# Optimization experiments

Measured on AMD Instinct MI355X. Metric: run time of the kernel, lower is better.

Reference implementation:

```python
import jax, jax.numpy as jnp
import numpy as np

NH, NG, NR = 128, 32, 15
NT, NS = 730, 800


def _linear_init(k, fan_in, fan_out):
    k1, k2 = jax.random.split(k)
    lim = 1.0 / np.sqrt(fan_in)
    w = jax.random.uniform(k1, (fan_in, fan_out), jnp.float32, -lim, lim)
    b = jax.random.uniform(k2, (fan_out,), jnp.float32, -lim, lim)
    return w, b


def _mlp(x, w1, b1, w2, b2):
    # Linear -> Tanh -> (Dropout: identity in eval) -> Linear
    return jnp.tanh(x @ w1 + b1) @ w2 + b2


def setup_inputs() -> dict:
    key = jax.random.key(0)
    ks = jax.random.split(key, 8)
    x = jax.random.normal(ks[0], (NT, NS, 6), jnp.float32)
    xc = jax.random.normal(ks[1], (NS, NG), jnp.float32)
    fcW1_w, fcW1_b = _linear_init(ks[2], NG, 256)
    fcW2_w, fcW2_b = _linear_init(ks[3], 256, NH * 7)
    fcT1_w, fcT1_b = _linear_init(ks[4], 6 + NG, 256)
    fcT2_w, fcT2_b = _linear_init(ks[5], 256, NH * 3)
    fcR1_w, fcR1_b = _linear_init(ks[6], NG, 256)
    fcR2_w, fcR2_b = _linear_init(ks[7], 256, NH * NR)
    return dict(x=x, xc=xc,
                fcW1_w=fcW1_w, fcW1_b=fcW1_b, fcW2_w=fcW2_w, fcW2_b=fcW2_b,
                fcT1_w=fcT1_w, fcT1_b=fcT1_b, fcT2_w=fcT2_w, fcT2_b=fcT2_b,
                fcR1_w=fcR1_w, fcR1_b=fcR1_b, fcR2_w=fcR2_w, fcR2_b=fcR2_b)


def _waternet(x, xc, fcW1_w, fcW1_b, fcW2_w, fcW2_b,
              fcT1_w, fcT1_b, fcT2_w, fcT2_b, fcR1_w, fcR1_b, fcR2_w, fcR2_b):
    nh, nr = NH, NR
    nt, ns, _ = x.shape
    P, E, T1, T2 = x[..., 0], x[..., 1], x[..., 2], x[..., 3]

    # static parameter head: [ns, nh*7] split into 7 physical params (sepPar)
    w = _mlp(xc, fcW1_w, fcW1_b, fcW2_w, fcW2_b)
    sig = jax.nn.sigmoid
    kp = sig(w[:, 0 * nh:1 * nh])
    ks_ = sig(w[:, 1 * nh:2 * nh])
    kg = sig(w[:, 2 * nh:3 * nh]) / 10.0
    gp = sig(w[:, 3 * nh:4 * nh])
    gL = jnp.exp(w[:, 4 * nh:5 * nh]) * 2.0
    qb = jax.nn.relu(w[:, 5 * nh:6 * nh])
    ga = jax.nn.softmax(w[:, 6 * nh:7 * nh], axis=1)

    # time-varying head on [forcings ; tiled static attrs]
    xcT = jnp.concatenate([x, jnp.broadcast_to(xc[None], (nt, ns, xc.shape[-1]))], axis=-1)
    v = _mlp(xcT, fcT1_w, fcT1_b, fcT2_w, fcT2_b)  # [nt, ns, nh*3]
    # vi = hardsigmoid(2*v) = clip((2v+3)/6, 0, 1) = clip(v/3 + 0.5, 0, 1)
    vi = jnp.clip(v[..., :nh] / 3.0 + 0.5, 0.0, 1.0)
    ve = jax.nn.relu(v[..., nh:2 * nh]) * 2.0
    vm = jnp.exp(v[..., 2 * nh:3 * nh])

    wR = _mlp(xc, fcR1_w, fcR1_b, fcR2_w, fcR2_b)  # [ns, nh*nr]

    # snow fraction vf = arccos((T1+T2)/(T2-T1))/pi, clamped by temperature masks
    denom = T2 - T1
    cf = (T1 + T2) / jnp.where(denom == 0.0, 1.0, denom)
    vf = jnp.arccos(jnp.clip(cf, -0.999999, 0.999999)) / 3.1415
    vf = jnp.where(T1 >= 0.0, 0.0, vf)
    vf = jnp.where(T2 <= 0.0, 1.0, vf)

    Ps = P * vf                                 # [nt, ns] snow
    Pl = (P * (1.0 - vf))[..., None] * vi       # [nt, ns, nh] liquid
    Ev = E[..., None] * ve                      # [nt, ns, nh]

    def step(carry, inp):
        Sf, Ss, Sg = carry
        ps, pl, ev, vmk = inp
        qf = jnp.minimum(Sf + ps[:, None], vmk)
        Sf = jax.nn.relu(Sf + ps[:, None] - vmk)
        H = jax.nn.relu(Ss + pl + qf - ev)
        qp = jax.nn.relu(kp * (H - gL))
        qs = ks_ * jnp.minimum(H, gL)
        Ss = H - qp - qs
        qsg = qs * gp
        qg = kg * (Sg + qsg) + qb
        Sg = Sg - qg
        # routing conv and final ga-sum are linear, so route qp+qso+qg together
        return (Sf, Ss, Sg), qp + qs * (1.0 - gp) + qg

    z = jnp.zeros((ns, nh), x.dtype)
    _, QT = jax.lax.scan(step, (z, z, z), (Ps, Pl, Ev, vm))  # QT: [nt, ns, nh]

    # convTS: per-(site, bucket) causal FIR routing with kernel r [ns, nh, nr]
    r = jax.nn.relu(wR).reshape(ns, nh, nr)
    xpad = jnp.pad(QT, ((nr - 1, 0), (0, 0), (0, 0)))
    QR = jnp.zeros_like(QT)
    for i in range(nr):  # small fixed nr taps
        QR = QR + xpad[nr - 1 - i:nr - 1 - i + nt] * r[:, :, i]

    return jnp.sum(QR * ga, axis=2)  # [nt, ns]


def reference(x, xc, fcW1_w, fcW1_b, fcW2_w, fcW2_b,
              fcT1_w, fcT1_b, fcT2_w, fcT2_b, fcR1_w, fcR1_b, fcR2_w, fcR2_b):
    return _waternet(x, xc, fcW1_w, fcW1_b, fcW2_w, fcW2_b,
                     fcT1_w, fcT1_b, fcT2_w, fcT2_b, fcR1_w, fcR1_b, fcR2_w, fcR2_b)
```

## Files before the change

### kernel.cpp

```cpp
#include <hip/hip_runtime.h>
#include <cmath>

#define NHID 128
#define NSITE 800
#define NTIME 730
#define NRTAP 15
constexpr int NSH = NSITE * NHID;

typedef _Float16 f16x8 __attribute__((ext_vector_type(8)));
typedef _Float16 f16x2 __attribute__((ext_vector_type(2)));
typedef float f32x4 __attribute__((ext_vector_type(4)));

__device__ __forceinline__ float tanh_fast(float x) {
    float e = __expf(2.0f * x);
    return 1.0f - 2.0f / (e + 1.0f);
}
__device__ __forceinline__ float sigmoid_fast(float x) {
    return 1.0f / (1.0f + __expf(-x));
}
__device__ __forceinline__ unsigned short h_bits(_Float16 h) {
    union { _Float16 h; unsigned short u; } c; c.h = h; return c.u;
}
__device__ __forceinline__ void unpack_h2(unsigned u, float& a, float& b) {
    union { unsigned u; f16x2 h; } cv; cv.u = u;
    a = (float)cv.h.x; b = (float)cv.h.y;
}
__device__ __forceinline__ int ah_swz(int jg, int r) {
    return jg * 64 + ((r & ~7) | ((r ^ jg) & 7));
}

__global__ void k_prep_w2h(const float* __restrict__ w2, _Float16* __restrict__ w2s)
{
    int idx = blockIdx.x * 256 + threadIdx.x;
    if (idx >= 98304) return;
    int k = idx / 384, col = idx - k * 384;
    int K0 = k >> 5, kg = (k >> 3) & 3, e = k & 7;
    w2s[(size_t)K0 * 12288 + kg * 3072 + col * 8 + e] = (_Float16)w2[(size_t)k * 384 + col];
}

__global__ void k_site_l1(const float* __restrict__ xc,
                          const float* __restrict__ w1W, const float* __restrict__ b1W,
                          const float* __restrict__ w1R, const float* __restrict__ b1R,
                          const float* __restrict__ w1T, const float* __restrict__ b1T,
                          float* __restrict__ h1w, float* __restrict__ h1r,
                          float* __restrict__ basec)
{
    __shared__ float xr[32];
    int s = blockIdx.x, j = threadIdx.x;
    if (j < 32) xr[j] = xc[s * 32 + j];
    __syncthreads();
    float aW = b1W[j], aR = b1R[j], aT = b1T[j];
#pragma unroll 8
    for (int k = 0; k < 32; ++k) {
        float xv = xr[k];
        aW = fmaf(xv, w1W[k * 256 + j], aW);
        aR = fmaf(xv, w1R[k * 256 + j], aR);
        aT = fmaf(xv, w1T[(6 + k) * 256 + j], aT);
    }
    h1w[s * 256 + j]   = tanh_fast(aW);
    h1r[s * 256 + j]   = tanh_fast(aR);
    basec[s * 256 + j] = aT;
}

__global__ void k_whead(const float* __restrict__ h1w,
                        const float* __restrict__ w2, const float* __restrict__ b2,
                        float* __restrict__ params)
{
    __shared__ float h[8 * 256];
    int sBase = blockIdx.x * 8, g = blockIdx.y, tid = threadIdx.x;
    for (int p = tid; p < 2048; p += 128) h[p] = h1w[sBase * 256 + p];
    __syncthreads();
    float bias = b2[g * 128 + tid];
    float acc[8];
#pragma unroll
    for (int i = 0; i < 8; ++i) acc[i] = bias;
    for (int k = 0; k < 256; ++k) {
        float wv = w2[k * 896 + g * 128 + tid];
#pragma unroll
        for (int i = 0; i < 8; ++i) acc[i] = fmaf(h[i * 256 + k], wv, acc[i]);
    }
#pragma unroll
    for (int i = 0; i < 8; ++i) {
        float v = acc[i], o;
        if (g == 0 || g == 1 || g == 3)  o = sigmoid_fast(v);
        else if (g == 2)                 o = sigmoid_fast(v) * 0.1f;
        else if (g == 4)                 o = __expf(v) * 2.0f;
        else if (g == 5)                 o = fmaxf(v, 0.0f);
        else                             o = v;
        params[g * NSH + (sBase + i) * 128 + tid] = o;
    }
}

__global__ void k_softmax_ga(float* __restrict__ ga)
{
    int s = blockIdx.x, h = threadIdx.x;
    float v = ga[s * 128 + h];
    float m = v;
#pragma unroll
    for (int off = 32; off; off >>= 1) m = fmaxf(m, __shfl_xor(m, off));
    __shared__ float ra[2], rb[2];
    if ((h & 63) == 0) ra[h >> 6] = m;
    __syncthreads();
    m = fmaxf(ra[0], ra[1]);
    float e = __expf(v - m);
    float t = e;
#pragma unroll
    for (int off = 32; off; off >>= 1) t += __shfl_xor(t, off);
    if ((h & 63) == 0) rb[h >> 6] = t;
    __syncthreads();
    ga[s * 128 + h] = e / (rb[0] + rb[1]);
}

__global__ void k_rhead(const float* __restrict__ h1r,
                        const float* __restrict__ w2, const float* __restrict__ b2,
                        float* __restrict__ rbuf)
{
    __shared__ float h[8 * 256];
    int sBase = blockIdx.x * 8, g = blockIdx.y, tid = threadIdx.x;
    for (int p = tid; p < 2048; p += 128) h[p] = h1r[sBase * 256 + p];
    __syncthreads();
    int c = g * 128 + tid;
    float bias = b2[c];
    float acc[8];
#pragma unroll
    for (int i = 0; i < 8; ++i) acc[i] = bias;
    for (int k = 0; k < 256; ++k) {
        float wv = w2[k * 1920 + c];
#pragma unroll
        for (int i = 0; i < 8; ++i) acc[i] = fmaf(h[i * 256 + k], wv, acc[i]);
    }
    int hh = c / 15, ii = c - hh * 15;
#pragma unroll
    for (int i = 0; i < 8; ++i)
        rbuf[ii * NSH + (sBase + i) * 128 + hh] = fmaxf(acc[i], 0.0f);
}

struct ThSm3 {
    f16x8 Ah[2048];
    float xt[64][6];
    float pls[64], evs[64], psv[64];
};

__global__ __launch_bounds__(512, 2) void k_combo6(
    const float* __restrict__ x, const float* __restrict__ w1T,
    const float* __restrict__ basec, const f16x8* __restrict__ w2B,
    const float* __restrict__ b2,
    const float* __restrict__ params, const float* __restrict__ rbuf,
    float* __restrict__ state, float* __restrict__ fut, float* __restrict__ out,
    unsigned* __restrict__ PVw, float* __restrict__ PSw, int t0h, int rowsH,
    const unsigned* __restrict__ PVr, const float* __restrict__ PSr,
    int t0s, int Tcs, int isFirst, int nScan)
{
    __shared__ __align__(16) char smem[sizeof(ThSm3)];
    int tid = threadIdx.x;

    if ((int)blockIdx.x < nScan) {
        float* part = (float*)smem;
        int sl = tid >> 7, hc = tid & 127;
        int lane = tid & 63, wid = tid >> 6;
        int site = blockIdx.x * 4 + sl;
        int cell = site * 128 + hc;

        float kp  = params[0 * NSH + cell];
        float ksP = params[1 * NSH + cell];
        float kgP = params[2 * NSH + cell];
        float gp  = params[3 * NSH + cell];
        float gL  = params[4 * NSH + cell];
        float qb  = params[5 * NSH + cell];
        float ga  = params[6 * NSH + cell];
        float kq  = ksP * (1.0f - gp);

        float wr[NRTAP];
#pragma unroll
        for (int i = 0; i < NRTAP; ++i) wr[i] = ga * rbuf[i * NSH + cell];

        float Sf, Ss, Sg, f[NRTAP];
        if (isFirst) {
            Sf = Ss = Sg = 0.0f;
#pragma unroll
            for (int i = 0; i < NRTAP; ++i) f[i] = 0.0f;
        } else {
            Sf = state[cell];
            Ss = state[NSH + cell];
            Sg = state[2 * NSH + cell];
#pragma unroll
            for (int i = 0; i < NRTAP; ++i) f[i] = fut[i * NSH + cell];
        }

        const unsigned* pvp = PVr + cell;

#define LD_T(PV_, PS_, T_) { int t_ = (T_); bool ok_ = t_ < Tcs;               \
        PV_ = ok_ ? pvp[(size_t)t_ * NSH] : 0u;                                \
        PS_ = ok_ ? PSr[(size_t)t_ * 800 + site] : 0.0f; }

        unsigned pvA[4], pvB[4], pvC[4], pvD[4];
        float psA[4], psB[4], psC[4], psD[4];
#pragma unroll
        for (int i = 0; i < 4; ++i) LD_T(pvA[i], psA[i], i)
#pragma unroll
        for (int i = 0; i < 4; ++i) LD_T(pvB[i], psB[i], 4 + i)
#pragma unroll
        for (int i = 0; i < 4; ++i) LD_T(pvC[i], psC[i], 8 + i)
#pragma unroll
        for (int i = 0; i < 4; ++i) LD_T(pvD[i], psD[i], 12 + i)

        int ngroups = (Tcs + 3) >> 2;
        for (int g = 0; g < ngroups; ++g) {
            int tb = g * 4;
            unsigned pvE[4]; float psE[4];
#pragma unroll
            for (int i = 0; i < 4; ++i) LD_T(pvE[i], psE[i], tb + 16 + i)

            float cs[4];
#pragma unroll
            for (int i = 0; i < 4; ++i) {
                cs[i] = 0.0f;
                if (tb + i < Tcs) {
                    float dlt, vm;
                    unpack_h2(pvA[i], dlt, vm);
                    float ps = psA[i];

                    float x1 = Sf + ps;
                    float qf = fminf(x1, vm);
                    Sf = fmaxf(x1 - vm, 0.0f);
                    float H  = fmaxf(Ss + qf + dlt, 0.0f);
                    float qp = fmaxf(kp * (H - gL), 0.0f);
                    float mh = fminf(H, gL);
                    float qs = ksP * mh;
                    Ss = H - qp - qs;
                    float qg = fmaf(kgP, fmaf(qs, gp, Sg), qb);
                    Sg = Sg - qg;
                    float qt = qp + kq * mh + qg;
#pragma unroll
                    for (int j = 0; j < NRTAP; ++j) f[j] = fmaf(wr[j], qt, f[j]);
                    cs[i] = f[0];
#pragma unroll
                    for (int j = 0; j < NRTAP - 1; ++j) f[j] = f[j + 1];
                    f[NRTAP - 1] = 0.0f;
                }
            }
#pragma unroll
            for (int i = 0; i < 4; ++i) {
                float c = cs[i];
#pragma unroll
                for (int off = 32; off; off >>= 1) c += __shfl_xor(c, off);
                cs[i] = c;
            }
            if (lane == 0) {
#pragma unroll
                for (int i = 0; i < 4; ++i)
                    if (tb + i < Tcs) part[wid * 128 + tb + i] = cs[i];
            }
#pragma unroll
            for (int i = 0; i < 4; ++i) {
                pvA[i] = pvB[i]; pvB[i] = pvC[i]; pvC[i] = pvD[i]; pvD[i] = pvE[i];
                psA[i] = psB[i]; psB[i] = psC[i]; psC[i] = psD[i]; psD[i] = psE[i];
            }
        }
#undef LD_T

        state[cell]           = Sf;
        state[NSH + cell]     = Ss;
        state[2 * NSH + cell] = Sg;
#pragma unroll
        for (int i = 0; i < NRTAP; ++i) fut[i * NSH + cell] = f[i];

        __syncthreads();
        {
            int sl2 = tid >> 7, tl = tid & 127;
            for (int t = tl; t < Tcs; t += 128)
                out[(size_t)(t0s + t) * 800 + blockIdx.x * 4 + sl2] =
                    part[(sl2 * 2) * 128 + t] + part[(sl2 * 2 + 1) * 128 + t];
        }
        return;
    }

    ThSm3* sm = (ThSm3*)smem;
    int m0 = ((int)blockIdx.x - nScan) * 64;
    int wid = tid >> 6, lane = tid & 63;
    int l15 = lane & 15, l4 = lane >> 4;
    int n0w = wid * 16;

    if (tid < 64) {
        int row = m0 + tid;
        const float* xp = &x[((size_t)t0h * 800 + row) * 6];
        float P = xp[0], E = xp[1], T1 = xp[2], T2 = xp[3];
        sm->xt[tid][0] = P;  sm->xt[tid][1] = E;     sm->xt[tid][2] = T1;
        sm->xt[tid][3] = T2; sm->xt[tid][4] = xp[4]; sm->xt[tid][5] = xp[5];
        float den = T2 - T1;
        float cf = (T1 + T2) / ((den == 0.0f) ? 1.0f : den);
        cf = fminf(fmaxf(cf, -0.999999f), 0.999999f);
        float vf = acosf(cf) * (1.0f / 3.1415f);
        vf = (T1 >= 0.0f) ? 0.0f : vf;
        vf = (T2 <= 0.0f) ? 1.0f : vf;
        sm->pls[tid] = P * (1.0f - vf);
        sm->evs[tid] = E;
        sm->psv[tid] = P * vf;
        PSw[row] = P * vf;
    }
    __syncthreads();

    {
        int jg = tid & 31, rg = tid >> 5;
        int j0 = jg * 8;
        float4 wA[6], wB[6];
#pragma unroll
        for (int c = 0; c < 6; ++c) {
            wA[c] = *(const float4*)&w1T[c * 256 + j0];
            wB[c] = *(const float4*)&w1T[c * 256 + j0 + 4];
        }
#pragma unroll
        for (int rr = 0; rr < 4; ++rr) {
            int r = rg * 4 + rr;
            int srow = (m0 + r) % 800;
            const float* bp = &basec[(size_t)srow * 256 + j0];
            float4 b0 = *(const float4*)bp;
            float4 b1 = *(const float4*)(bp + 4);
            float a[8] = {b0.x, b0.y, b0.z, b0.w, b1.x, b1.y, b1.z, b1.w};
#pragma unroll
            for (int c = 0; c < 6; ++c) {
                float xv = sm->xt[r][c];
                a[0] = fmaf(xv, wA[c].x, a[0]);
                a[1] = fmaf(xv, wA[c].y, a[1]);
                a[2] = fmaf(xv, wA[c].z, a[2]);
                a[3] = fmaf(xv, wA[c].w, a[3]);
                a[4] = fmaf(xv, wB[c].x, a[4]);
                a[5] = fmaf(xv, wB[c].y, a[5]);
                a[6] = fmaf(xv, wB[c].z, a[6]);
                a[7] = fmaf(xv, wB[c].w, a[7]);
            }
            f16x8 hv;
#pragma unroll
            for (int e = 0; e < 8; ++e) hv[e] = (_Float16)tanh_fast(a[e]);
            sm->Ah[ah_swz(jg, r)] = hv;
        }
    }
    __syncthreads();

    f32x4 acc[4][3];
#pragma unroll
    for (int ch = 0; ch < 3; ++ch) {
        float bb = b2[ch * 128 + n0w + l15];
#pragma unroll
        for (int mf = 0; mf < 4; ++mf) acc[mf][ch] = (f32x4){bb, bb, bb, bb};
    }
    f16x8 bf[3], bfn[3];
#pragma unroll
    for (int ch = 0; ch < 3; ++ch)
        bf[ch] = w2B[(size_t)l4 * 384 + ch * 128 + n0w + l15];
    for (int ks = 0; ks < 8; ++ks) {
        if (ks < 7) {
#pragma unroll
            for (int ch = 0; ch < 3; ++ch)
                bfn[ch] = w2B[(size_t)(ks + 1) * 1536 + l4 * 384 + ch * 128 + n0w + l15];
        }
        f16x8 af[4];
#pragma unroll
        for (int mf = 0; mf < 4; ++mf)
            af[mf] = sm->Ah[ah_swz(ks * 4 + l4, mf * 16 + l15)];
#pragma unroll
        for (int mf = 0; mf < 4; ++mf)
#pragma unroll
            for (int ch = 0; ch < 3; ++ch)
                acc[mf][ch] = __builtin_amdgcn_mfma_f32_16x16x32_f16(
                    af[mf], bf[ch], acc[mf][ch], 0, 0, 0);
        if (ks < 7) {
#pragma unroll
            for (int ch = 0; ch < 3; ++ch) bf[ch] = bfn[ch];
        }
    }

    int col = n0w + l15;
#pragma unroll
    for (int mf = 0; mf < 4; ++mf) {
#pragma unroll
        for (int rr = 0; rr < 4; ++rr) {
            int r = mf * 16 + l4 * 4 + rr;
            float vp = acc[mf][0][rr];
            float ve = acc[mf][1][rr];
            float vv = acc[mf][2][rr];
            float opl = sm->pls[r] * fminf(fmaxf(vp * (1.0f / 3.0f) + 0.5f, 0.0f), 1.0f);
            float oev = sm->evs[r] * fmaxf(ve, 0.0f) * 2.0f;
            float dlt = opl - oev;
            float ovm = fminf(__expf(vv), 60000.0f);
            unsigned pv = (unsigned)h_bits((_Float16)dlt)
                        | ((unsigned)h_bits((_Float16)ovm) << 16);
            PVw[(size_t)(m0 + r) * 128 + col] = pv;
        }
    }
}

extern "C" void kernel_launch(void* const* d_in, const int* in_sizes, int n_in,
                              void* d_out, int out_size, void* d_ws, size_t ws_size,
                              hipStream_t stream)
{
    const float* x      = (const float*)d_in[0];
    const float* xc     = (const float*)d_in[1];
    const float* fcW1_w = (const float*)d_in[2];
    const float* fcW1_b = (const float*)d_in[3];
    const float* fcW2_w = (const float*)d_in[4];
    const float* fcW2_b = (const float*)d_in[5];
    const float* fcT1_w = (const float*)d_in[6];
    const float* fcT1_b = (const float*)d_in[7];
    const float* fcT2_w = (const float*)d_in[8];
    const float* fcT2_b = (const float*)d_in[9];
    const float* fcR1_w = (const float*)d_in[10];
    const float* fcR1_b = (const float*)d_in[11];
    const float* fcR2_w = (const float*)d_in[12];
    const float* fcR2_b = (const float*)d_in[13];
    float* out = (float*)d_out;

    char* wsb = (char*)d_ws;
    size_t off = 0;
    float* params = (float*)(wsb + off); off += (size_t)7 * NSH * 4;
    float* rbuf   = (float*)(wsb + off); off += (size_t)NRTAP * NSH * 4;
    float* basec  = (float*)(wsb + off); off += 800 * 256 * 4;
    float* h1w    = (float*)(wsb + off); off += 800 * 256 * 4;
    float* h1r    = (float*)(wsb + off); off += 800 * 256 * 4;
    float* state  = (float*)(wsb + off); off += (size_t)3 * NSH * 4;
    float* fut    = (float*)(wsb + off); off += (size_t)NRTAP * NSH * 4;
    _Float16* w2s = (_Float16*)(wsb + off); off += 98304 * 2;
    size_t fixedB = off;

    const size_t perT = (size_t)NSH * 4 + 800 * 4;
    long avail = (long)ws_size - (long)fixedB - 4096;
    int Tc = (int)(avail / (long)(2 * perT));
    if (Tc > 128) Tc = 128;
    Tc &= ~3;
    if (Tc < 4) Tc = 4;

    unsigned* PV0 = (unsigned*)(wsb + off); off += (size_t)Tc * NSH * 4;
    float*    PS0 = (float*)(wsb + off);    off += (size_t)Tc * 800 * 4;
    unsigned* PV1 = (unsigned*)(wsb + off); off += (size_t)Tc * NSH * 4;
    float*    PS1 = (float*)(wsb + off);    off += (size_t)Tc * 800 * 4;

    k_prep_w2h<<<384, 256, 0, stream>>>(fcT2_w, w2s);
    k_site_l1<<<800, 256, 0, stream>>>(xc, fcW1_w, fcW1_b, fcR1_w, fcR1_b,
                                       fcT1_w, fcT1_b, h1w, h1r, basec);
    k_whead<<<dim3(100, 7), 128, 0, stream>>>(h1w, fcW2_w, fcW2_b, params);
    k_softmax_ga<<<800, 128, 0, stream>>>(params + (size_t)6 * NSH);
    k_rhead<<<dim3(100, 15), 128, 0, stream>>>(h1r, fcR2_w, fcR2_b, rbuf);

    int nch = (NTIME + Tc - 1) / Tc;
    for (int c = 0; c <= nch; ++c) {
        int nScan = (c > 0) ? 200 : 0;
        int Tch = 0;
        if (c < nch) { Tch = NTIME - c * Tc; if (Tch > Tc) Tch = Tc; }
        int rowsH = Tch * 800;
        int thB = rowsH / 64;
        int grid = nScan + thB;
        if (grid == 0) continue;
        int t0s = (c - 1) * Tc;
        int Tcs = 0;
        if (c > 0) { Tcs = NTIME - t0s; if (Tcs > Tc) Tcs = Tc; }
        unsigned* PVw = (c & 1) ? PV1 : PV0;
        float*    PSw = (c & 1) ? PS1 : PS0;
        const unsigned* PVr = ((c - 1) & 1) ? PV1 : PV0;
        const float*    PSr = ((c - 1) & 1) ? PS1 : PS0;
        k_combo6<<<grid, 512, 0, stream>>>(
            x, fcT1_w, basec, (const f16x8*)w2s, fcT2_b, params, rbuf,
            state, fut, out,
            PVw, PSw, c * Tc, rowsH,
            PVr, PSr, t0s, Tcs, (c == 1) ? 1 : 0, nScan);
    }
}
```

Measured before the change: 458.6 us.

## Fold parameter heads into first combo launch and use fixed uneven chunk schedule

Removes the separate whead, softmax and rhead launches and runs them as extra block roles inside the first time-head launch of the combo kernel, with the softmax fused into the whead role. Uses a fixed chunk schedule with a small tail chunk, and pads the PV/PS buffers so the scan's lookahead loads no longer need bounds checks. Scan blocks raise their wave priority so the serial recurrence is favoured over co-resident time-head blocks. This cuts launch overhead and the pipeline-fill cost, at the price of more workspace and unguarded reads of padding data that are never consumed.

```diff
diff --git a/kernel.cpp b/kernel.cpp
--- a/kernel.cpp
+++ b/kernel.cpp
@@ -5,6 +5,9 @@
 #define NSITE 800
 #define NTIME 730
 #define NRTAP 15
+#define NCH 7
+#define TCMAX 128
+#define TPAD 24
 constexpr int NSH = NSITE * NHID;
 
 typedef _Float16 f16x8 __attribute__((ext_vector_type(8)));
@@ -62,103 +65,35 @@
     basec[s * 256 + j] = aT;
 }
 
-__global__ void k_whead(const float* __restrict__ h1w,
-                        const float* __restrict__ w2, const float* __restrict__ b2,
-                        float* __restrict__ params)
-{
-    __shared__ float h[8 * 256];
-    int sBase = blockIdx.x * 8, g = blockIdx.y, tid = threadIdx.x;
-    for (int p = tid; p < 2048; p += 128) h[p] = h1w[sBase * 256 + p];
-    __syncthreads();
-    float bias = b2[g * 128 + tid];
-    float acc[8];
-#pragma unroll
-    for (int i = 0; i < 8; ++i) acc[i] = bias;
-    for (int k = 0; k < 256; ++k) {
-        float wv = w2[k * 896 + g * 128 + tid];
-#pragma unroll
-        for (int i = 0; i < 8; ++i) acc[i] = fmaf(h[i * 256 + k], wv, acc[i]);
-    }
-#pragma unroll
-    for (int i = 0; i < 8; ++i) {
-        float v = acc[i], o;
-        if (g == 0 || g == 1 || g == 3)  o = sigmoid_fast(v);
-        else if (g == 2)                 o = sigmoid_fast(v) * 0.1f;
-        else if (g == 4)                 o = __expf(v) * 2.0f;
-        else if (g == 5)                 o = fmaxf(v, 0.0f);
-        else                             o = v;
-        params[g * NSH + (sBase + i) * 128 + tid] = o;
-    }
-}
-
-__global__ void k_softmax_ga(float* __restrict__ ga)
-{
-    int s = blockIdx.x, h = threadIdx.x;
-    float v = ga[s * 128 + h];
-    float m = v;
-#pragma unroll
-    for (int off = 32; off; off >>= 1) m = fmaxf(m, __shfl_xor(m, off));
-    __shared__ float ra[2], rb[2];
-    if ((h & 63) == 0) ra[h >> 6] = m;
-    __syncthreads();
-    m = fmaxf(ra[0], ra[1]);
-    float e = __expf(v - m);
-    float t = e;
-#pragma unroll
-    for (int off = 32; off; off >>= 1) t += __shfl_xor(t, off);
-    if ((h & 63) == 0) rb[h >> 6] = t;
-    __syncthreads();
-    ga[s * 128 + h] = e / (rb[0] + rb[1]);
-}
-
-__global__ void k_rhead(const float* __restrict__ h1r,
-                        const float* __restrict__ w2, const float* __restrict__ b2,
-                        float* __restrict__ rbuf)
-{
-    __shared__ float h[8 * 256];
-    int sBase = blockIdx.x * 8, g = blockIdx.y, tid = threadIdx.x;
-    for (int p = tid; p < 2048; p += 128) h[p] = h1r[sBase * 256 + p];
-    __syncthreads();
-    int c = g * 128 + tid;
-    float bias = b2[c];
-    float acc[8];
-#pragma unroll
-    for (int i = 0; i < 8; ++i) acc[i] = bias;
-    for (int k = 0; k < 256; ++k) {
-        float wv = w2[k * 1920 + c];
-#pragma unroll
-        for (int i = 0; i < 8; ++i) acc[i] = fmaf(h[i * 256 + k], wv, acc[i]);
-    }
-    int hh = c / 15, ii = c - hh * 15;
-#pragma unroll
-    for (int i = 0; i < 8; ++i)
-        rbuf[ii * NSH + (sBase + i) * 128 + hh] = fmaxf(acc[i], 0.0f);
-}
-
 struct ThSm3 {
     f16x8 Ah[2048];
     float xt[64][6];
     float pls[64], evs[64], psv[64];
 };
 
-__global__ __launch_bounds__(512, 2) void k_combo6(
+__global__ __launch_bounds__(512, 2) void k_combo7(
     const float* __restrict__ x, const float* __restrict__ w1T,
     const float* __restrict__ basec, const f16x8* __restrict__ w2B,
     const float* __restrict__ b2,
-    const float* __restrict__ params, const float* __restrict__ rbuf,
+    float* __restrict__ params, float* __restrict__ rbuf,
     float* __restrict__ state, float* __restrict__ fut, float* __restrict__ out,
     unsigned* __restrict__ PVw, float* __restrict__ PSw, int t0h, int rowsH,
     const unsigned* __restrict__ PVr, const float* __restrict__ PSr,
-    int t0s, int Tcs, int isFirst, int nScan)
+    int t0s, int Tcs, int isFirst, int nScan, int nWh, int nRh,
+    const float* __restrict__ h1w, const float* __restrict__ h1r,
+    const float* __restrict__ w2W, const float* __restrict__ b2W,
+    const float* __restrict__ w2R, const float* __restrict__ b2R)
 {
     __shared__ __align__(16) char smem[sizeof(ThSm3)];
     int tid = threadIdx.x;
-
-    if ((int)blockIdx.x < nScan) {
+    int bid = (int)blockIdx.x;
+
+    if (bid < nScan) {
+        __builtin_amdgcn_s_setprio(1);
         float* part = (float*)smem;
         int sl = tid >> 7, hc = tid & 127;
         int lane = tid & 63, wid = tid >> 6;
-        int site = blockIdx.x * 4 + sl;
+        int site = bid * 4 + sl;
         int cell = site * 128 + hc;
 
         float kp  = params[0 * NSH + cell];
@@ -189,9 +124,9 @@
 
         const unsigned* pvp = PVr + cell;
 
-#define LD_T(PV_, PS_, T_) { int t_ = (T_); bool ok_ = t_ < Tcs;               \
-        PV_ = ok_ ? pvp[(size_t)t_ * NSH] : 0u;                                \
-        PS_ = ok_ ? PSr[(size_t)t_ * 800 + site] : 0.0f; }
+#define LD_T(PV_, PS_, T_) { int t_ = (T_);                                    \
+        PV_ = pvp[(size_t)t_ * NSH];                                           \
+        PS_ = PSr[(size_t)t_ * 800 + site]; }
 
         unsigned pvA[4], pvB[4], pvC[4], pvD[4];
         float psA[4], psB[4], psC[4], psD[4];
@@ -258,6 +193,7 @@
             }
         }
 #undef LD_T
+        __builtin_amdgcn_s_setprio(0);
 
         state[cell]           = Sf;
         state[NSH + cell]     = Ss;
@@ -269,14 +205,112 @@
         {
             int sl2 = tid >> 7, tl = tid & 127;
             for (int t = tl; t < Tcs; t += 128)
-                out[(size_t)(t0s + t) * 800 + blockIdx.x * 4 + sl2] =
+                out[(size_t)(t0s + t) * 800 + bid * 4 + sl2] =
                     part[(sl2 * 2) * 128 + t] + part[(sl2 * 2 + 1) * 128 + t];
         }
         return;
     }
 
+    if (bid < nScan + nWh) {
+        int bidh = bid - nScan;
+        int ublk = tid >> 7, utid = tid & 127;
+        int g = bidh / 25;
+        int sBase = ((bidh % 25) * 4 + ublk) * 8;
+        float* hb  = (float*)smem + ublk * 2048;
+        float* red = (float*)smem + 8192;
+
+        for (int p = utid; p < 2048; p += 128) hb[p] = h1w[sBase * 256 + p];
+        __syncthreads();
+
+        float bias = b2W[g * 128 + utid];
+        float acc[8];
+#pragma unroll
+        for (int i = 0; i < 8; ++i) acc[i] = bias;
+        for (int k = 0; k < 256; ++k) {
+            float wv = w2W[k * 896 + g * 128 + utid];
+#pragma unroll
+            for (int i = 0; i < 8; ++i) acc[i] = fmaf(hb[i * 256 + k], wv, acc[i]);
+        }
+        if (g != 6) {
+#pragma unroll
+            for (int i = 0; i < 8; ++i) {
+                float v = acc[i], o;
+                if (g == 0 || g == 1 || g == 3)  o = sigmoid_fast(v);
+                else if (g == 2)                 o = sigmoid_fast(v) * 0.1f;
+                else if (g == 4)                 o = __expf(v) * 2.0f;
+                else                             o = fmaxf(v, 0.0f);
+                params[g * NSH + (sBase + i) * 128 + utid] = o;
+            }
+        } else {
+            int w2i = ublk * 2 + (utid >> 6);
+            float m[8];
+#pragma unroll
+            for (int i = 0; i < 8; ++i) m[i] = acc[i];
+#pragma unroll
+            for (int off = 32; off; off >>= 1)
+#pragma unroll
+                for (int i = 0; i < 8; ++i) m[i] = fmaxf(m[i], __shfl_xor(m[i], off));
+            if ((utid & 63) == 0) {
+#pragma unroll
+                for (int i = 0; i < 8; ++i) red[w2i * 8 + i] = m[i];
+            }
+            __syncthreads();
+#pragma unroll
+            for (int i = 0; i < 8; ++i)
+                m[i] = fmaxf(red[(ublk * 2) * 8 + i], red[(ublk * 2 + 1) * 8 + i]);
+            float e[8], sm_[8];
+#pragma unroll
+            for (int i = 0; i < 8; ++i) { e[i] = __expf(acc[i] - m[i]); sm_[i] = e[i]; }
+#pragma unroll
+            for (int off = 32; off; off >>= 1)
+#pragma unroll
+                for (int i = 0; i < 8; ++i) sm_[i] += __shfl_xor(sm_[i], off);
+            __syncthreads();
+            if ((utid & 63) == 0) {
+#pragma unroll
+                for (int i = 0; i < 8; ++i) red[w2i * 8 + i] = sm_[i];
+            }
+            __syncthreads();
+#pragma unroll
+            for (int i = 0; i < 8; ++i) {
+                float tot = red[(ublk * 2) * 8 + i] + red[(ublk * 2 + 1) * 8 + i];
+                params[6 * NSH + (sBase + i) * 128 + utid] = e[i] / tot;
+            }
+        }
+        return;
+    }
+
+    if (bid < nScan + nWh + nRh) {
+        int bidr = bid - nScan - nWh;
+        int ublk = tid >> 7, utid = tid & 127;
+        int unit = bidr * 4 + ublk;
+        int g2 = unit % 15;
+        int sBase = (unit / 15) * 8;
+        float* hb = (float*)smem + ublk * 2048;
+
+        for (int p = utid; p < 2048; p += 128) hb[p] = h1r[sBase * 256 + p];
+        __syncthreads();
+
+        int c2 = g2 * 128 + utid;
+        float bias = b2R[c2];
+        float acc[8];
+#pragma unroll
+        for (int i = 0; i < 8; ++i) acc[i] = bias;
+        for (int k = 0; k < 256; ++k) {
+            float wv = w2R[k * 1920 + c2];
+#pragma unroll
+            for (int i = 0; i < 8; ++i) acc[i] = fmaf(hb[i * 256 + k], wv, acc[i]);
+        }
+        int hh = c2 / 15, ii = c2 - hh * 15;
+#pragma unroll
+        for (int i = 0; i < 8; ++i)
+            rbuf[ii * NSH + (sBase + i) * 128 + hh] = fmaxf(acc[i], 0.0f);
+        return;
+    }
+
     ThSm3* sm = (ThSm3*)smem;
-    int m0 = ((int)blockIdx.x - nScan) * 64;
+    int m0 = (bid - nScan - nWh - nRh) * 64;
+    if (m0 >= rowsH) return;
     int wid = tid >> 6, lane = tid & 63;
     int l15 = lane & 15, l4 = lane >> 4;
     int n0w = wid * 16;
@@ -420,47 +454,42 @@
     float* state  = (float*)(wsb + off); off += (size_t)3 * NSH * 4;
     float* fut    = (float*)(wsb + off); off += (size_t)NRTAP * NSH * 4;
     _Float16* w2s = (_Float16*)(wsb + off); off += 98304 * 2;
-    size_t fixedB = off;
-
-    const size_t perT = (size_t)NSH * 4 + 800 * 4;
-    long avail = (long)ws_size - (long)fixedB - 4096;
-    int Tc = (int)(avail / (long)(2 * perT));
-    if (Tc > 128) Tc = 128;
-    Tc &= ~3;
-    if (Tc < 4) Tc = 4;
-
-    unsigned* PV0 = (unsigned*)(wsb + off); off += (size_t)Tc * NSH * 4;
-    float*    PS0 = (float*)(wsb + off);    off += (size_t)Tc * 800 * 4;
-    unsigned* PV1 = (unsigned*)(wsb + off); off += (size_t)Tc * NSH * 4;
-    float*    PS1 = (float*)(wsb + off);    off += (size_t)Tc * 800 * 4;
+
+    const int TBUF = TCMAX + TPAD;
+    unsigned* PV0 = (unsigned*)(wsb + off); off += (size_t)TBUF * NSH * 4;
+    float*    PS0 = (float*)(wsb + off);    off += (size_t)TBUF * 800 * 4;
+    unsigned* PV1 = (unsigned*)(wsb + off); off += (size_t)TBUF * NSH * 4;
+    float*    PS1 = (float*)(wsb + off);    off += (size_t)TBUF * 800 * 4;
+
+    const int csz[NCH]   = {128, 128, 128, 128, 128, 72, 18};
+    int cstart[NCH];
+    { int a = 0; for (int i = 0; i < NCH; ++i) { cstart[i] = a; a += csz[i]; } }
 
     k_prep_w2h<<<384, 256, 0, stream>>>(fcT2_w, w2s);
     k_site_l1<<<800, 256, 0, stream>>>(xc, fcW1_w, fcW1_b, fcR1_w, fcR1_b,
                                        fcT1_w, fcT1_b, h1w, h1r, basec);
-    k_whead<<<dim3(100, 7), 128, 0, stream>>>(h1w, fcW2_w, fcW2_b, params);
-    k_softmax_ga<<<800, 128, 0, stream>>>(params + (size_t)6 * NSH);
-    k_rhead<<<dim3(100, 15), 128, 0, stream>>>(h1r, fcR2_w, fcR2_b, rbuf);
-
-    int nch = (NTIME + Tc - 1) / Tc;
-    for (int c = 0; c <= nch; ++c) {
+
+    for (int c = 0; c <= NCH; ++c) {
         int nScan = (c > 0) ? 200 : 0;
-        int Tch = 0;
-        if (c < nch) { Tch = NTIME - c * Tc; if (Tch > Tc) Tch = Tc; }
+        int nWh   = (c == 0) ? 175 : 0;
+        int nRh   = (c == 0) ? 375 : 0;
+        int Tch = (c < NCH) ? csz[c] : 0;
         int rowsH = Tch * 800;
         int thB = rowsH / 64;
-        int grid = nScan + thB;
+        int grid = nScan + nWh + nRh + thB;
         if (grid == 0) continue;
-        int t0s = (c - 1) * Tc;
-        int Tcs = 0;
-        if (c > 0) { Tcs = NTIME - t0s; if (Tcs > Tc) Tcs = Tc; }
+        int t0h = (c < NCH) ? cstart[c] : 0;
+        int t0s = (c > 0) ? cstart[c - 1] : 0;
+        int Tcs = (c > 0) ? csz[c - 1] : 0;
         unsigned* PVw = (c & 1) ? PV1 : PV0;
         float*    PSw = (c & 1) ? PS1 : PS0;
         const unsigned* PVr = ((c - 1) & 1) ? PV1 : PV0;
         const float*    PSr = ((c - 1) & 1) ? PS1 : PS0;
-        k_combo6<<<grid, 512, 0, stream>>>(
+        k_combo7<<<grid, 512, 0, stream>>>(
             x, fcT1_w, basec, (const f16x8*)w2s, fcT2_b, params, rbuf,
             state, fut, out,
-            PVw, PSw, c * Tc, rowsH,
-            PVr, PSr, t0s, Tcs, (c == 1) ? 1 : 0, nScan);
-    }
-}
+            PVw, PSw, t0h, rowsH,
+            PVr, PSr, t0s, Tcs, (c == 1) ? 1 : 0, nScan, nWh, nRh,
+            h1w, h1r, fcW2_w, fcW2_b, fcR2_w, fcR2_b);
+    }
+}
```

Measured after the change: 423.3 us. -7.7%, faster.
